# Performance work log

Hardware: AMD Instinct MI355X
Metric: run time of the kernel (lower is better)

The kernel has to match this reference:

```python
import jax, jax.numpy as jnp
import numpy as np

EPS = 1e-6
D_MODEL, D_HEAD, COND_F = 1024, 64, 768
N_HEADS = D_MODEL // D_HEAD
BATCH, SEQ = 2, 2048


def _rope_freqs(d_head, n_heads):
    # RoPE.__init__: dim = d_head // 2; count = n_heads * dim // 4 = n_heads * d_head // 8
    d8 = d_head // 8
    log_min, log_max = np.log(np.pi), np.log(10.0 * np.pi)
    f = np.exp(np.linspace(log_min, log_max, n_heads * d8 + 1, dtype=np.float64)[:-1])
    return jnp.asarray(f.reshape(d8, n_heads).T, dtype=jnp.float32)  # [nh, d8]


def _apply_rotary(x, theta):
    # x: [n, nh, l, e], theta: [n, nh, l, d8]; rotate first 2*d8 channels
    d = theta.shape[-1]
    x1, x2, rest = x[..., :d], x[..., d:2 * d], x[..., 2 * d:]
    cos, sin = jnp.cos(theta), jnp.sin(theta)
    y1 = x1 * cos - x2 * sin
    y2 = x2 * cos + x1 * sin
    return jnp.concatenate([y1, y2, rest], axis=-1)


def setup_inputs() -> dict:
    key = jax.random.key(0)
    ks = jax.random.split(key, 6)
    x = jax.random.normal(ks[0], (BATCH, SEQ, D_MODEL), dtype=jnp.float32)
    pos = jnp.broadcast_to(jnp.arange(SEQ, dtype=jnp.float32), (BATCH, SEQ))[..., None]
    cond = jax.random.normal(ks[1], (BATCH, COND_F), dtype=jnp.float32)
    w_norm = jax.random.normal(ks[2], (D_MODEL, COND_F), dtype=jnp.float32) * 0.02
    w_qkv = jax.random.normal(ks[3], (3 * D_MODEL, D_MODEL), dtype=jnp.float32) * 0.02
    scale = jnp.full((N_HEADS,), 10.0, dtype=jnp.float32)
    w_out = jax.random.normal(ks[4], (D_MODEL, D_MODEL), dtype=jnp.float32) * 0.02
    return {"x": x, "pos": pos, "cond": cond, "w_norm": w_norm,
            "w_qkv": w_qkv, "scale": scale, "w_out": w_out}


def reference(x, pos, cond, w_norm, w_qkv, scale, w_out):
    n, l, d = x.shape
    nh, e = N_HEADS, D_HEAD
    skip = x
    # AdaRMSNorm: scale = (linear(cond) + 1) * rsqrt(mean(x^2))
    cond_scale = cond @ w_norm.T + 1.0                      # [n, d]
    mean_sq = jnp.mean(x * x, axis=-1, keepdims=True)       # [n, l, 1]
    xn = x * (cond_scale[:, None, :] * jax.lax.rsqrt(mean_sq + EPS))
    # QKV projection
    qkv = (xn @ w_qkv.T).reshape(n, l, 3, nh, e)
    q = jnp.transpose(qkv[:, :, 0], (0, 2, 1, 3))           # [n, nh, l, e]
    k = jnp.transpose(qkv[:, :, 1], (0, 2, 1, 3))
    v = jnp.transpose(qkv[:, :, 2], (0, 2, 1, 3))
    # cosine-sim scaling
    sqrt_scale = jnp.sqrt(scale)[None, :, None, None]       # [1, nh, 1, 1]
    q = q * (sqrt_scale * jax.lax.rsqrt(jnp.sum(q * q, axis=-1, keepdims=True) + EPS))
    k = k * (sqrt_scale * jax.lax.rsqrt(jnp.sum(k * k, axis=-1, keepdims=True) + EPS))
    # RoPE: theta = pos[..., None] * freqs -> [n, l, nh, d8] -> [n, nh, l, d8]
    freqs = _rope_freqs(e, nh)
    theta = jnp.transpose(pos[..., None] * freqs, (0, 2, 1, 3))
    q = _apply_rotary(q, theta)
    k = _apply_rotary(k, theta)
    # attention with softmax scale = 1.0
    scores = jnp.einsum('nhle,nhme->nhlm', q, k)
    attn = jax.nn.softmax(scores, axis=-1)
    out = jnp.einsum('nhlm,nhme->nhle', attn, v)
    out = jnp.transpose(out, (0, 2, 1, 3)).reshape(n, l, d)
    return out @ w_out.T + skip
```

## Files before the change

kernel.cpp:

```cpp
#include <hip/hip_runtime.h>
#include <math.h>

#define D_MODEL 1024
#define D_HEAD  64
#define N_HEADS 16
#define COND_F  768
#define BATCH   2
#define SEQ     2048
#define NTOK    (BATCH*SEQ)
#define QKV_N   (3*D_MODEL)

typedef unsigned short u16;
typedef __attribute__((ext_vector_type(4))) float  f32x4;
typedef __attribute__((ext_vector_type(8))) __bf16 bfrag;
typedef __attribute__((ext_vector_type(4))) unsigned short u16x4;
typedef __attribute__((ext_vector_type(8))) unsigned short u16x8;

__device__ __forceinline__ u16 f2bf(float f) {
    unsigned u = __builtin_bit_cast(unsigned, f);
    return (u16)((u + 0x7fffu + ((u >> 16) & 1u)) >> 16);
}
__device__ __forceinline__ float bf2f(u16 h) {
    unsigned u = ((unsigned)h) << 16;
    return __builtin_bit_cast(float, u);
}

__device__ __forceinline__ float fexp2(float x) {
    float y;
    asm("v_exp_f32 %0, %1" : "=v"(y) : "v"(x));
    return y;
}

__device__ __forceinline__ void async16(const void* g, void* l) {
    __builtin_amdgcn_global_load_lds(
        (const __attribute__((address_space(1))) unsigned int*)g,
        (__attribute__((address_space(3))) unsigned int*)l, 16, 0, 0);
}

#define SBAR do { __builtin_amdgcn_sched_barrier(0); \
                  __builtin_amdgcn_s_barrier(); \
                  __builtin_amdgcn_sched_barrier(0); } while (0)
#define WAITV3 do { asm volatile("s_waitcnt vmcnt(3)" ::: "memory"); } while (0)
#define WAITV2 do { asm volatile("s_waitcnt vmcnt(2)" ::: "memory"); } while (0)
#define WAITV0 do { asm volatile("s_waitcnt vmcnt(0)" ::: "memory"); } while (0)

__global__ __launch_bounds__(256) void prep_kernel(const float* __restrict__ wqkv,
                                                   const float* __restrict__ wout,
                                                   u16* __restrict__ wqkv_b,
                                                   u16* __restrict__ wout_b,
                                                   const float* __restrict__ cond,
                                                   const float* __restrict__ w_norm,
                                                   float* __restrict__ cs,
                                                   const float* __restrict__ pos,
                                                   float2* __restrict__ tab) {
    if (blockIdx.x < 2048) {
        int i = blockIdx.x * 256 + threadIdx.x;
        const int n1 = QKV_N * D_MODEL / 8;
        const float* src; u16* dst; int off;
        if (i < n1) { src = wqkv; dst = wqkv_b; off = i * 8; }
        else        { src = wout; dst = wout_b; off = (i - n1) * 8; }
        float4 a = *(const float4*)(src + off);
        float4 b = *(const float4*)(src + off + 4);
        *(u16x4*)(dst + off)     = (u16x4){f2bf(a.x), f2bf(a.y), f2bf(a.z), f2bf(a.w)};
        *(u16x4*)(dst + off + 4) = (u16x4){f2bf(b.x), f2bf(b.y), f2bf(b.z), f2bf(b.w)};
    } else if (blockIdx.x < 2560) {
        int lane = threadIdx.x & 63, w = threadIdx.x >> 6;
        int wid = (blockIdx.x - 2048) * 4 + w;
        int b = wid >> 10, d = wid & 1023;
        const float* c = cond + b * COND_F;
        const float* wn = w_norm + (size_t)d * COND_F;
        float acc = 0.f;
        #pragma unroll
        for (int kk = 0; kk < 3; ++kk) {
            int j = kk * 256 + lane * 4;
            float4 cv = *(const float4*)(c + j);
            float4 wv = *(const float4*)(wn + j);
            acc += cv.x * wv.x + cv.y * wv.y + cv.z * wv.z + cv.w * wv.w;
        }
        for (int m = 1; m < 64; m <<= 1) acc += __shfl_xor(acc, m);
        if (lane == 0) cs[wid] = acc + 1.0f;
    } else {
        int i = (blockIdx.x - 2560) * 256 + threadIdx.x;
        int j = i & 7, h = (i >> 3) & 15;
        int s = i >> 7;
        double lf = 1.1447298858494001741 + (double)(j * 16 + h) * (2.302585092994045684 / 128.0);
        float fr = (float)exp(lf);
        float th = pos[s] * fr;
        tab[i] = make_float2(cosf(th), sinf(th));
    }
}

__global__ __launch_bounds__(256) void rmsnorm_kernel(const float* __restrict__ x,
                                                      const float* __restrict__ cs,
                                                      u16* __restrict__ xn) {
    int tok = blockIdx.x, t = threadIdx.x;
    int b = tok >> 11;
    const float* xr = x + (size_t)tok * D_MODEL;
    float4 v = *(const float4*)(xr + t * 4);
    float ss = v.x * v.x + v.y * v.y + v.z * v.z + v.w * v.w;
    for (int m = 1; m < 64; m <<= 1) ss += __shfl_xor(ss, m);
    __shared__ float red[4];
    int w = t >> 6;
    if ((t & 63) == 0) red[w] = ss;
    __syncthreads();
    float tot = red[0] + red[1] + red[2] + red[3];
    float r = rsqrtf(tot * (1.0f / D_MODEL) + 1e-6f);
    float4 cv = *(const float4*)(cs + b * D_MODEL + t * 4);
    *(u16x4*)(xn + (size_t)tok * D_MODEL + t * 4) =
        (u16x4){f2bf(v.x * cv.x * r), f2bf(v.y * cv.y * r),
                f2bf(v.z * cv.z * r), f2bf(v.w * cv.w * r)};
}

__global__ __launch_bounds__(512) void gemm_qkv(const u16* __restrict__ A, const u16* __restrict__ B,
                                                u16* __restrict__ Cq, u16* __restrict__ Ck,
                                                u16* __restrict__ Cv,
                                                const float* __restrict__ scale,
                                                const float2* __restrict__ tab,
                                                int M, int N, int K) {
    __shared__ u16 As0[128 * 32];
    __shared__ u16 As1[128 * 32];
    __shared__ u16 As2[128 * 32];
    __shared__ u16 Bs0[128 * 32];
    __shared__ u16 Bs1[128 * 32];
    __shared__ u16 Bs2[128 * 32];
    int tid = threadIdx.x;
    int lane = tid & 63, w = tid >> 6;
    int wr = w >> 1, wc = w & 1;
    int m0 = blockIdx.x * 128, n0 = blockIdx.y * 128;
    f32x4 acc[2][4] = {};
    const u16* Ag = A + (size_t)m0 * K;
    const u16* Bg = B + (size_t)n0 * K;
    int lr = lane & 15, lq = lane >> 4;

    int srow = tid >> 2, scol = (tid & 3) * 8;

    #define GSTAGE(kt, Ad, Bd) do { \
        async16(Ag + (size_t)srow * K + (kt) + scol, Ad + tid * 8); \
        async16(Bg + (size_t)srow * K + (kt) + scol, Bd + tid * 8); } while (0)

    auto compute = [&](const u16* Asb, const u16* Bsb) {
        bfrag af[2], bfv[4];
        #pragma unroll
        for (int fm = 0; fm < 2; ++fm)
            af[fm] = *(const bfrag*)&Asb[(wr * 32 + fm * 16 + lr) * 32 + lq * 8];
        #pragma unroll
        for (int fn = 0; fn < 4; ++fn)
            bfv[fn] = *(const bfrag*)&Bsb[(wc * 64 + fn * 16 + lr) * 32 + lq * 8];
        #pragma unroll
        for (int fm = 0; fm < 2; ++fm)
            #pragma unroll
            for (int fn = 0; fn < 4; ++fn)
                acc[fm][fn] = __builtin_amdgcn_mfma_f32_16x16x32_bf16(af[fm], bfv[fn], acc[fm][fn], 0, 0, 0);
    };

    const int NK = K / 32;
    GSTAGE(0, As0, Bs0);
    GSTAGE(32, As1, Bs1);

    for (int t = 0; t < NK - 2; t += 3) {
        WAITV2; SBAR; GSTAGE((size_t)(t + 2) * 32, As2, Bs2); compute(As0, Bs0);
        WAITV2; SBAR; GSTAGE((size_t)(t + 3) * 32, As0, Bs0); compute(As1, Bs1);
        WAITV2; SBAR; GSTAGE((size_t)(t + 4) * 32, As1, Bs1); compute(As2, Bs2);
    }
    WAITV2; SBAR; compute(As0, Bs0);
    WAITV0; SBAR; compute(As1, Bs1);
    #undef GSTAGE

    int colbase0 = n0 + wc * 64;
    int sel = colbase0 >> 10;
    int h = (colbase0 >> 6) & 15;
    int bb = m0 >> 11;
    if (sel == 2) {
        #pragma unroll
        for (int fm = 0; fm < 2; ++fm) {
            int sP = (m0 & 2047) + wr * 32 + 8 * lq + 4 * fm;
            #pragma unroll
            for (int fn = 0; fn < 4; ++fn) {
                int e = fn * 16 + lr;
                u16x4 pk = {f2bf(acc[fm][fn][0]), f2bf(acc[fm][fn][1]),
                            f2bf(acc[fm][fn][2]), f2bf(acc[fm][fn][3])};
                *(u16x4*)&Cv[((size_t)(bb * N_HEADS + h) * D_HEAD + e) * SEQ + sP] = pk;
            }
        }
    } else {
        u16* p = sel ? Ck : Cq;
        float sq = sqrtf(scale[h]);
        float mult = (sel == 0) ? sq * 1.4426950408889634f : sq;
        #pragma unroll
        for (int fm = 0; fm < 2; ++fm) {
            int s0 = (m0 & 2047) + wr * 32 + fm * 16 + lq * 4;
            #pragma unroll
            for (int r = 0; r < 4; ++r) {
                float v0 = acc[fm][0][r], v1 = acc[fm][1][r],
                      v2 = acc[fm][2][r], v3 = acc[fm][3][r];
                float ss = v0 * v0 + v1 * v1 + v2 * v2 + v3 * v3;
                ss += __shfl_xor(ss, 1); ss += __shfl_xor(ss, 2);
                ss += __shfl_xor(ss, 4); ss += __shfl_xor(ss, 8);
                float rs = mult * rsqrtf(ss + 1e-6f);
                v0 *= rs; v1 *= rs; v2 *= rs; v3 *= rs;
                float part = __shfl_xor(v0, 8);
                float2 cs2 = tab[((size_t)(s0 + r) * 16 + h) * 8 + (lr & 7)];
                v0 = (lr < 8) ? v0 * cs2.x - part * cs2.y
                              : v0 * cs2.x + part * cs2.y;
                size_t rp = ((size_t)(bb * N_HEADS + h) * SEQ + (s0 + r)) * D_HEAD;
                p[rp + lr]      = f2bf(v0);
                p[rp + 16 + lr] = f2bf(v1);
                p[rp + 32 + lr] = f2bf(v2);
                p[rp + 48 + lr] = f2bf(v3);
            }
        }
    }
}

__global__ __launch_bounds__(256) void gemm_out(const u16* __restrict__ A, const u16* __restrict__ B,
                                                float* __restrict__ Cf,
                                                const float* __restrict__ skip,
                                                int M, int N, int K) {
    __shared__ u16 As0[128 * 32];
    __shared__ u16 As1[128 * 32];
    __shared__ u16 As2[128 * 32];
    __shared__ u16 Bs0[64 * 32];
    __shared__ u16 Bs1[64 * 32];
    __shared__ u16 Bs2[64 * 32];
    int tid = threadIdx.x;
    int lane = tid & 63, w = tid >> 6;
    int m0 = blockIdx.x * 128, n0 = blockIdx.y * 64;
    f32x4 acc[2][4] = {};
    const u16* Ag = A + (size_t)m0 * K;
    const u16* Bg = B + (size_t)n0 * K;
    int lr = lane & 15, lq = lane >> 4;

    int c1 = 256 + tid;

    #define GSTAGE(kt, Ad, Bd) do { \
        async16(Ag + (size_t)(tid >> 2) * K + (kt) + (tid & 3) * 8, Ad + tid * 8); \
        async16(Ag + (size_t)(c1 >> 2) * K + (kt) + (c1 & 3) * 8, Ad + c1 * 8); \
        async16(Bg + (size_t)(tid >> 2) * K + (kt) + (tid & 3) * 8, Bd + tid * 8); } while (0)

    auto compute = [&](const u16* Asb, const u16* Bsb) {
        bfrag af[2], bfv[4];
        #pragma unroll
        for (int fm = 0; fm < 2; ++fm)
            af[fm] = *(const bfrag*)&Asb[(w * 32 + fm * 16 + lr) * 32 + lq * 8];
        #pragma unroll
        for (int fn = 0; fn < 4; ++fn)
            bfv[fn] = *(const bfrag*)&Bsb[(fn * 16 + lr) * 32 + lq * 8];
        #pragma unroll
        for (int fm = 0; fm < 2; ++fm)
            #pragma unroll
            for (int fn = 0; fn < 4; ++fn)
                acc[fm][fn] = __builtin_amdgcn_mfma_f32_16x16x32_bf16(af[fm], bfv[fn], acc[fm][fn], 0, 0, 0);
    };

    const int NK = K / 32;
    GSTAGE(0, As0, Bs0);
    GSTAGE(32, As1, Bs1);

    for (int t = 0; t < NK - 2; t += 3) {
        WAITV3; SBAR; GSTAGE((size_t)(t + 2) * 32, As2, Bs2); compute(As0, Bs0);
        WAITV3; SBAR; GSTAGE((size_t)(t + 3) * 32, As0, Bs0); compute(As1, Bs1);
        WAITV3; SBAR; GSTAGE((size_t)(t + 4) * 32, As1, Bs1); compute(As2, Bs2);
    }
    WAITV3; SBAR; compute(As0, Bs0);
    WAITV0; SBAR; compute(As1, Bs1);
    #undef GSTAGE

    #pragma unroll
    for (int fm = 0; fm < 2; ++fm) {
        int rowbase = m0 + w * 32 + fm * 16 + lq * 4;
        #pragma unroll
        for (int fn = 0; fn < 4; ++fn) {
            int col = n0 + fn * 16 + lr;
            #pragma unroll
            for (int r = 0; r < 4; ++r) {
                int row = rowbase + r;
                Cf[(size_t)row * N + col] = acc[fm][fn][r] + skip[(size_t)row * N + col];
            }
        }
    }
}

__global__ __launch_bounds__(512) void attn_kernel(const u16* __restrict__ q,
                                                   const u16* __restrict__ k,
                                                   const u16* __restrict__ vt,
                                                   u16* __restrict__ o_part,
                                                   float* __restrict__ lsum_part) {
    __shared__ u16 Ks0[64 * 64];
    __shared__ u16 Ks1[64 * 64];
    __shared__ u16 Vs0[64 * 64];
    __shared__ u16 Vs1[64 * 64];
    int tid = threadIdx.x, lane = tid & 63, w = tid >> 6;

    int rid = blockIdx.x;
    int nwg = gridDim.x, cpx = nwg >> 3;
    int wid = (rid & 7) * cpx + (rid >> 3);
    int xq = wid & 7;
    int rest = wid >> 3;
    int bh = rest & 31;
    int z = rest >> 5;
    int nz = nwg >> 8;
    int qs = xq * 256;
    int chunk = SEQ / nz;
    int kv0 = z * chunk;
    int lr = lane & 15, lq = lane >> 4;

    bfrag qf[2][2];
    #pragma unroll
    for (int mf = 0; mf < 2; ++mf) {
        const u16* qb = q + ((size_t)bh * SEQ + qs + w * 32 + mf * 16 + lr) * D_HEAD + lq * 8;
        qf[mf][0] = *(const bfrag*)qb;
        qf[mf][1] = *(const bfrag*)(qb + 32);
    }
    bfrag ones;
    #pragma unroll
    for (int j = 0; j < 8; ++j) ones[j] = (__bf16)1.0f;

    f32x4 oacc[2][4] = {};
    f32x4 oacc5[2] = {};
    const u16* kbase = k + (size_t)bh * SEQ * D_HEAD;
    const u16* vbase = vt + (size_t)bh * D_HEAD * SEQ;

    int srow = tid >> 3, scol = (tid & 7) ^ ((tid >> 3) & 7);
    const u16* kg = kbase + (size_t)srow * 64 + scol * 8;
    const u16* vg = vbase + (size_t)srow * SEQ + scol * 8;

    #define STAGE(kt, Kd, Vd) do { \
        async16(kg + (size_t)(kt) * 64, Kd + tid * 8); \
        async16(vg + (kt),              Vd + tid * 8); } while (0)

    auto tile_compute = [&](const u16* Kb, const u16* Vb) {
        f32x4 sacc[2][4] = {};
        __builtin_amdgcn_s_setprio(1);
        #pragma unroll
        for (int nb = 0; nb < 4; ++nb) {
            int row = nb * 16 + lr;
            #pragma unroll
            for (int kb = 0; kb < 2; ++kb) {
                bfrag kf = *(const bfrag*)&Kb[row * 64 + (((kb * 4 + lq) ^ (row & 7)) * 8)];
                sacc[0][nb] = __builtin_amdgcn_mfma_f32_16x16x32_bf16(kf, qf[0][kb], sacc[0][nb], 0, 0, 0);
                sacc[1][nb] = __builtin_amdgcn_mfma_f32_16x16x32_bf16(kf, qf[1][kb], sacc[1][nb], 0, 0, 0);
            }
        }
        __builtin_amdgcn_s_setprio(0);

        #pragma unroll
        for (int kb = 0; kb < 2; ++kb) {
            bfrag pf[2];
            #pragma unroll
            for (int mf = 0; mf < 2; ++mf)
                #pragma unroll
                for (int half = 0; half < 2; ++half) {
                    int nb = kb * 2 + half;
                    #pragma unroll
                    for (int r = 0; r < 4; ++r)
                        pf[mf][half * 4 + r] = (__bf16)fexp2(sacc[mf][nb][r]);
                }
            __builtin_amdgcn_s_setprio(1);
            oacc5[0] = __builtin_amdgcn_mfma_f32_16x16x32_bf16(pf[0], ones, oacc5[0], 0, 0, 0);
            oacc5[1] = __builtin_amdgcn_mfma_f32_16x16x32_bf16(pf[1], ones, oacc5[1], 0, 0, 0);
            #pragma unroll
            for (int eb = 0; eb < 4; ++eb) {
                int row = eb * 16 + lr;
                bfrag vf = *(const bfrag*)&Vb[row * 64 + (((kb * 4 + lq) ^ (row & 7)) * 8)];
                oacc[0][eb] = __builtin_amdgcn_mfma_f32_16x16x32_bf16(pf[0], vf, oacc[0][eb], 0, 0, 0);
                oacc[1][eb] = __builtin_amdgcn_mfma_f32_16x16x32_bf16(pf[1], vf, oacc[1][eb], 0, 0, 0);
            }
            __builtin_amdgcn_s_setprio(0);
        }
    };

    STAGE(kv0, Ks0, Vs0);
    asm volatile("s_waitcnt vmcnt(0)" ::: "memory");
    __syncthreads();

    const int NTILE = chunk / 64;
    for (int t = 0; t < NTILE; t += 2) {
        if (t + 1 < NTILE) STAGE(kv0 + (t + 1) * 64, Ks1, Vs1);
        tile_compute(Ks0, Vs0);
        __syncthreads();
        if (t + 2 < NTILE) STAGE(kv0 + (t + 2) * 64, Ks0, Vs0);
        if (t + 1 < NTILE) {
            tile_compute(Ks1, Vs1);
            __syncthreads();
        }
    }
    #undef STAGE

    int b = bh >> 4, h = bh & 15;
    u16* op = o_part + (size_t)z * NTOK * D_MODEL;
    #pragma unroll
    for (int mf = 0; mf < 2; ++mf) {
        #pragma unroll
        for (int r = 0; r < 4; ++r) {
            int qrow = qs + w * 32 + mf * 16 + lq * 4 + r;
            if (lr == 0)
                lsum_part[((size_t)z * BATCH * N_HEADS + bh) * SEQ + qrow] = oacc5[mf][r];
            #pragma unroll
            for (int eb = 0; eb < 4; ++eb) {
                int e = eb * 16 + lr;
                op[((size_t)b * SEQ + qrow) * D_MODEL + h * D_HEAD + e] = f2bf(oacc[mf][eb][r]);
            }
        }
    }
}

__global__ __launch_bounds__(256) void combine_kernel(const u16* __restrict__ o_part,
                                                      const float* __restrict__ lsum_part,
                                                      u16* __restrict__ out, int Z) {
    int i = blockIdx.x * 256 + threadIdx.x;
    int base = i * 8;
    int t = base >> 10, col = base & 1023;
    int b = t >> 11, s = t & 2047, h = col >> 6;
    size_t li = (size_t)(b * N_HEADS + h) * SEQ + s;
    float lsum = 0.f;
    for (int z = 0; z < Z; ++z) lsum += lsum_part[(size_t)z * BATCH * N_HEADS * SEQ + li];
    float inv = 1.0f / lsum;
    float acc[8] = {};
    for (int z = 0; z < Z; ++z) {
        u16x8 a = *(const u16x8*)(o_part + (size_t)z * NTOK * D_MODEL + base);
        #pragma unroll
        for (int j = 0; j < 8; ++j) acc[j] += bf2f(a[j]);
    }
    u16x8 r;
    #pragma unroll
    for (int j = 0; j < 8; ++j) r[j] = f2bf(acc[j] * inv);
    *(u16x8*)(out + base) = r;
}

extern "C" void kernel_launch(void* const* d_in, const int* in_sizes, int n_in,
                              void* d_out, int out_size, void* d_ws, size_t ws_size,
                              hipStream_t stream) {
    const float* x      = (const float*)d_in[0];
    const float* pos    = (const float*)d_in[1];
    const float* cond   = (const float*)d_in[2];
    const float* w_norm = (const float*)d_in[3];
    const float* w_qkv  = (const float*)d_in[4];
    const float* scale  = (const float*)d_in[5];
    const float* w_out  = (const float*)d_in[6];
    float* out = (float*)d_out;

    char* ws = (char*)d_ws;
    u16* xn     = (u16*)ws;
    u16* wqkv_b = (u16*)(ws + (8u  << 20));
    u16* wout_b = (u16*)(ws + (14u << 20));
    float* cs   = (float*)(ws + (16u << 20));
    u16* qb     = (u16*)(ws + (16u << 20) + (1u << 16));
    const size_t HSZ = (size_t)BATCH * N_HEADS * SEQ * D_HEAD;
    u16* kb = qb + HSZ;
    u16* vt = kb + HSZ;
    u16* o_part   = (u16*)(ws + (41u << 20));
    float2* tab   = (float2*)(ws + (41u << 20));
    u16* attn_o = xn;

    const int Z = 2;
    float* lsum_p = (float*)(ws + (41u << 20) + (size_t)Z * NTOK * D_MODEL * 2);

    prep_kernel<<<dim3(3584), dim3(256), 0, stream>>>(w_qkv, w_out, wqkv_b, wout_b,
                                                      cond, w_norm, cs, pos, (float2*)tab);
    rmsnorm_kernel<<<dim3(NTOK), dim3(256), 0, stream>>>(x, cs, xn);
    gemm_qkv<<<dim3(NTOK / 128, QKV_N / 128), dim3(512), 0, stream>>>(
        xn, wqkv_b, qb, kb, vt, scale, (const float2*)tab, NTOK, QKV_N, D_MODEL);
    attn_kernel<<<dim3(256 * Z), dim3(512), 0, stream>>>(
        qb, kb, vt, o_part, lsum_p);
    combine_kernel<<<dim3(NTOK * D_MODEL / 8 / 256), dim3(256), 0, stream>>>(o_part, lsum_p, attn_o, Z);
    gemm_out<<<dim3(NTOK / 128, D_MODEL / 64), dim3(256), 0, stream>>>(
        attn_o, wout_b, out, x, NTOK, D_MODEL, D_MODEL);
}
```

Measured before the change: 106.6 us.

## Drop split-KV attention and combine kernel; use 256-thread blocks over full sequence

Attention no longer splits the key/value range into two chunks with partial outputs. Each 256-thread block (4 waves) now handles 128 query rows over all 2048 keys and normalizes by the row sum in the epilogue. This removes the combine kernel launch and the round trip of partial outputs and sums through memory, and each thread now issues two async loads per K/V tile. The trade is a longer serial KV loop per block with the same 512-block grid, and fewer waves per block to hide latency.

```diff
diff --git a/kernel.cpp b/kernel.cpp
--- a/kernel.cpp
+++ b/kernel.cpp
@@ -280,11 +280,10 @@
     }
 }
 
-__global__ __launch_bounds__(512) void attn_kernel(const u16* __restrict__ q,
+__global__ __launch_bounds__(256) void attn_kernel(const u16* __restrict__ q,
                                                    const u16* __restrict__ k,
                                                    const u16* __restrict__ vt,
-                                                   u16* __restrict__ o_part,
-                                                   float* __restrict__ lsum_part) {
+                                                   u16* __restrict__ o) {
     __shared__ u16 Ks0[64 * 64];
     __shared__ u16 Ks1[64 * 64];
     __shared__ u16 Vs0[64 * 64];
@@ -294,14 +293,9 @@
     int rid = blockIdx.x;
     int nwg = gridDim.x, cpx = nwg >> 3;
     int wid = (rid & 7) * cpx + (rid >> 3);
-    int xq = wid & 7;
-    int rest = wid >> 3;
-    int bh = rest & 31;
-    int z = rest >> 5;
-    int nz = nwg >> 8;
-    int qs = xq * 256;
-    int chunk = SEQ / nz;
-    int kv0 = z * chunk;
+    int xq = wid & 15;
+    int bh = wid >> 4;
+    int qs = xq * 128;
     int lr = lane & 15, lq = lane >> 4;
 
     bfrag qf[2][2];
@@ -320,13 +314,19 @@
     const u16* kbase = k + (size_t)bh * SEQ * D_HEAD;
     const u16* vbase = vt + (size_t)bh * D_HEAD * SEQ;
 
-    int srow = tid >> 3, scol = (tid & 7) ^ ((tid >> 3) & 7);
-    const u16* kg = kbase + (size_t)srow * 64 + scol * 8;
-    const u16* vg = vbase + (size_t)srow * SEQ + scol * 8;
+    int c1t = tid + 256;
+    int sr0 = tid >> 3, sc0 = (tid & 7) ^ ((tid >> 3) & 7);
+    int sr1 = c1t >> 3, sc1 = (c1t & 7) ^ ((c1t >> 3) & 7);
+    const u16* kg0 = kbase + (size_t)sr0 * 64 + sc0 * 8;
+    const u16* kg1 = kbase + (size_t)sr1 * 64 + sc1 * 8;
+    const u16* vg0 = vbase + (size_t)sr0 * SEQ + sc0 * 8;
+    const u16* vg1 = vbase + (size_t)sr1 * SEQ + sc1 * 8;
 
     #define STAGE(kt, Kd, Vd) do { \
-        async16(kg + (size_t)(kt) * 64, Kd + tid * 8); \
-        async16(vg + (kt),              Vd + tid * 8); } while (0)
+        async16(kg0 + (size_t)(kt) * 64, Kd + tid * 8); \
+        async16(kg1 + (size_t)(kt) * 64, Kd + c1t * 8); \
+        async16(vg0 + (kt),              Vd + tid * 8); \
+        async16(vg1 + (kt),              Vd + c1t * 8); } while (0)
 
     auto tile_compute = [&](const u16* Kb, const u16* Vb) {
         f32x4 sacc[2][4] = {};
@@ -369,16 +369,16 @@
         }
     };
 
-    STAGE(kv0, Ks0, Vs0);
+    STAGE(0, Ks0, Vs0);
     asm volatile("s_waitcnt vmcnt(0)" ::: "memory");
     __syncthreads();
 
-    const int NTILE = chunk / 64;
+    const int NTILE = SEQ / 64;
     for (int t = 0; t < NTILE; t += 2) {
-        if (t + 1 < NTILE) STAGE(kv0 + (t + 1) * 64, Ks1, Vs1);
+        if (t + 1 < NTILE) STAGE((t + 1) * 64, Ks1, Vs1);
         tile_compute(Ks0, Vs0);
         __syncthreads();
-        if (t + 2 < NTILE) STAGE(kv0 + (t + 2) * 64, Ks0, Vs0);
+        if (t + 2 < NTILE) STAGE((t + 2) * 64, Ks0, Vs0);
         if (t + 1 < NTILE) {
             tile_compute(Ks1, Vs1);
             __syncthreads();
@@ -387,44 +387,19 @@
     #undef STAGE
 
     int b = bh >> 4, h = bh & 15;
-    u16* op = o_part + (size_t)z * NTOK * D_MODEL;
     #pragma unroll
     for (int mf = 0; mf < 2; ++mf) {
         #pragma unroll
         for (int r = 0; r < 4; ++r) {
+            float inv = 1.0f / oacc5[mf][r];
             int qrow = qs + w * 32 + mf * 16 + lq * 4 + r;
-            if (lr == 0)
-                lsum_part[((size_t)z * BATCH * N_HEADS + bh) * SEQ + qrow] = oacc5[mf][r];
             #pragma unroll
             for (int eb = 0; eb < 4; ++eb) {
                 int e = eb * 16 + lr;
-                op[((size_t)b * SEQ + qrow) * D_MODEL + h * D_HEAD + e] = f2bf(oacc[mf][eb][r]);
-            }
-        }
-    }
-}
-
-__global__ __launch_bounds__(256) void combine_kernel(const u16* __restrict__ o_part,
-                                                      const float* __restrict__ lsum_part,
-                                                      u16* __restrict__ out, int Z) {
-    int i = blockIdx.x * 256 + threadIdx.x;
-    int base = i * 8;
-    int t = base >> 10, col = base & 1023;
-    int b = t >> 11, s = t & 2047, h = col >> 6;
-    size_t li = (size_t)(b * N_HEADS + h) * SEQ + s;
-    float lsum = 0.f;
-    for (int z = 0; z < Z; ++z) lsum += lsum_part[(size_t)z * BATCH * N_HEADS * SEQ + li];
-    float inv = 1.0f / lsum;
-    float acc[8] = {};
-    for (int z = 0; z < Z; ++z) {
-        u16x8 a = *(const u16x8*)(o_part + (size_t)z * NTOK * D_MODEL + base);
-        #pragma unroll
-        for (int j = 0; j < 8; ++j) acc[j] += bf2f(a[j]);
-    }
-    u16x8 r;
-    #pragma unroll
-    for (int j = 0; j < 8; ++j) r[j] = f2bf(acc[j] * inv);
-    *(u16x8*)(out + base) = r;
+                o[((size_t)b * SEQ + qrow) * D_MODEL + h * D_HEAD + e] = f2bf(oacc[mf][eb][r] * inv);
+            }
+        }
+    }
 }
 
 extern "C" void kernel_launch(void* const* d_in, const int* in_sizes, int n_in,
@@ -448,21 +423,15 @@
     const size_t HSZ = (size_t)BATCH * N_HEADS * SEQ * D_HEAD;
     u16* kb = qb + HSZ;
     u16* vt = kb + HSZ;
-    u16* o_part   = (u16*)(ws + (41u << 20));
-    float2* tab   = (float2*)(ws + (41u << 20));
+    float2* tab = (float2*)(ws + (41u << 20));
     u16* attn_o = xn;
-
-    const int Z = 2;
-    float* lsum_p = (float*)(ws + (41u << 20) + (size_t)Z * NTOK * D_MODEL * 2);
 
     prep_kernel<<<dim3(3584), dim3(256), 0, stream>>>(w_qkv, w_out, wqkv_b, wout_b,
                                                       cond, w_norm, cs, pos, (float2*)tab);
     rmsnorm_kernel<<<dim3(NTOK), dim3(256), 0, stream>>>(x, cs, xn);
     gemm_qkv<<<dim3(NTOK / 128, QKV_N / 128), dim3(512), 0, stream>>>(
         xn, wqkv_b, qb, kb, vt, scale, (const float2*)tab, NTOK, QKV_N, D_MODEL);
-    attn_kernel<<<dim3(256 * Z), dim3(512), 0, stream>>>(
-        qb, kb, vt, o_part, lsum_p);
-    combine_kernel<<<dim3(NTOK * D_MODEL / 8 / 256), dim3(256), 0, stream>>>(o_part, lsum_p, attn_o, Z);
+    attn_kernel<<<dim3(512), dim3(256), 0, stream>>>(qb, kb, vt, attn_o);
     gemm_out<<<dim3(NTOK / 128, D_MODEL / 64), dim3(256), 0, stream>>>(
         attn_o, wout_b, out, x, NTOK, D_MODEL, D_MODEL);
 }
```

After: 108.1 us. No clear change (+1.4%).
